# Kernel optimization log

Hardware: AMD Instinct MI355X
Metric: run time of the kernel (lower is better)

Reference implementation:

```python
import jax, jax.numpy as jnp
import numpy as np

N_NODES = 100000


def gcn_conv(x, row, col, norm, W, b):
    # PyG GCNConv: linear transform first, then normalized aggregation.
    h = x @ W                                   # [N, D_out]
    msg = h[col] * norm[:, None]                # gather sources, scale  [E', D_out]
    out = jax.ops.segment_sum(msg, row, num_segments=N_NODES)
    return out + b


def _build_norm(edge_index, n):
    # add self-loops
    loops = jnp.arange(n, dtype=edge_index.dtype)
    row = jnp.concatenate([edge_index[0], loops])  # targets
    col = jnp.concatenate([edge_index[1], loops])  # sources
    deg = jax.ops.segment_sum(jnp.ones(row.shape[0], jnp.float32), row, num_segments=n)
    dinv = jnp.where(deg > 0, jax.lax.rsqrt(deg), 0.0)
    norm = dinv[row] * dinv[col]
    return row, col, norm


def setup_inputs() -> dict:
    key = jax.random.key(0)
    k = jax.random.split(key, 5)
    N, E, IN, H, OUT = N_NODES, 1_600_000, 128, 64, 64
    x = jax.random.normal(k[0], (N, IN), jnp.float32)
    edge_index = jax.random.randint(k[1], (2, E), 0, N, dtype=jnp.int32)
    W1 = jax.random.normal(k[2], (IN, H), jnp.float32) / np.sqrt(IN)
    b1 = jnp.zeros((H,), jnp.float32)
    W2 = jax.random.normal(k[3], (H, OUT), jnp.float32) / np.sqrt(H)
    b2 = jnp.zeros((OUT,), jnp.float32)
    return {"x": x, "edge_index": edge_index, "W1": W1, "b1": b1, "W2": W2, "b2": b2}


def reference(x, edge_index, W1, b1, W2, b2):
    row, col, norm = _build_norm(edge_index, N_NODES)
    h = jax.nn.relu(gcn_conv(x, row, col, norm, W1, b1))
    # dropout is identity in eval mode
    out = gcn_conv(h, row, col, norm, W2, b2)
    return out
```

## Files before the change

kernel.cpp:

```cpp
#include <hip/hip_runtime.h>
#include <hip/hip_bf16.h>
#include <stdint.h>


#define BUCKET_CAP 64
#define GATHER_CAP 58
#define NB_SHIFT 8
#define BIN_W (1 << NB_SHIFT)
#define EPB 4096

typedef __bf16 bf16x8 __attribute__((ext_vector_type(8)));
typedef float  f32x4  __attribute__((ext_vector_type(4)));

__device__ __forceinline__ void prep_w_one(const float* __restrict__ W,
                                           __bf16* __restrict__ Wsw, int t) {
    int lane = t & 63;
    int f = t >> 6;
    int kt = f >> 2, nt = f & 3;
    int k0 = kt * 32 + ((lane >> 4) * 8);
    int n  = nt * 16 + (lane & 15);
    __bf16* dst = Wsw + (size_t)t * 8;
#pragma unroll
    for (int j = 0; j < 8; ++j)
        dst[j] = (__bf16)W[(size_t)(k0 + j) * 64 + n];
}

__global__ void k_binA(const int* __restrict__ row, const int* __restrict__ col,
                       int E, int NB, int NBLK,
                       const float* __restrict__ W1, const float* __restrict__ W2,
                       __bf16* __restrict__ W1sw, __bf16* __restrict__ W2sw,
                       int* __restrict__ lofs_g, int* __restrict__ binbuf) {
    __shared__ int hist[512];
    __shared__ int lofs[512];
    __shared__ int cur[512];
    __shared__ int stage[EPB];
    __shared__ int wsum[4];
    int t = threadIdx.x;
    int blk = blockIdx.x;

    if (blk >= NBLK) {
        int b = blk - NBLK;
        if (b < 4)      prep_w_one(W1, W1sw, b * 256 + t);
        else if (b < 6) prep_w_one(W2, W2sw, (b - 4) * 256 + t);
        return;
    }

    int e0 = blk * EPB;
    int nE = E - e0; if (nE > EPB) nE = EPB;

    for (int i = t; i < 512; i += 256) hist[i] = 0;
    __syncthreads();

    int rr[EPB / 256], cc[EPB / 256];
#pragma unroll
    for (int k = 0; k < EPB / 256; ++k) {
        int idx = k * 256 + t;
        if (idx < nE) {
            rr[k] = row[e0 + idx];
            cc[k] = col[e0 + idx];
            atomicAdd(&hist[((unsigned)rr[k]) >> NB_SHIFT], 1);
        } else rr[k] = -1;
    }
    __syncthreads();

    int h0 = hist[2 * t], h1 = hist[2 * t + 1];
    int s = h0 + h1;
    int v = s;
#pragma unroll
    for (int off = 1; off < 64; off <<= 1) {
        int u = __shfl_up(v, off);
        if ((t & 63) >= off) v += u;
    }
    if ((t & 63) == 63) wsum[t >> 6] = v;
    __syncthreads();
    int wo = 0;
    for (int w = 0; w < (t >> 6); ++w) wo += wsum[w];
    int base = v + wo - s;
    lofs[2 * t]     = base;
    lofs[2 * t + 1] = base + h0;
    cur[2 * t]      = base;
    cur[2 * t + 1]  = base + h0;
    __syncthreads();

#pragma unroll
    for (int k = 0; k < EPB / 256; ++k) {
        if (rr[k] >= 0) {
            int b = ((unsigned)rr[k]) >> NB_SHIFT;
            int p = atomicAdd(&cur[b], 1);
            stage[p] = (cc[k] << NB_SHIFT) | (rr[k] & (BIN_W - 1));
        }
    }
    __syncthreads();

    for (int i = t; i < nE; i += 256)
        binbuf[(size_t)blk * EPB + i] = stage[i];
    for (int i = t; i <= NB; i += 256)
        lofs_g[(size_t)blk * (NB + 1) + i] = lofs[i];
}

#define BB_THREADS 512
__global__ void k_binB(const int* __restrict__ lofs_g, const int* __restrict__ binbuf,
                       int NBLK, int NB, int* __restrict__ cnt, float* __restrict__ dinv,
                       int* __restrict__ bucket, int N) {
    __shared__ int loc[BIN_W];
    int t = threadIdx.x;
    int k = blockIdx.x;
    int node0 = k << NB_SHIFT;

    for (int i = t; i < BIN_W; i += BB_THREADS) loc[i] = 0;
    __syncthreads();

    if (t < NBLK) {
        int s0 = lofs_g[(size_t)t * (NB + 1) + k];
        int s1 = lofs_g[(size_t)t * (NB + 1) + k + 1];
        const int* __restrict__ seg = binbuf + (size_t)t * EPB;
        int i = s0;
        int nxt = (i < s1) ? seg[i] : 0;
        while (i < s1) {
            int v = nxt;
            ++i;
            if (i < s1) nxt = seg[i];
            int rl = v & (BIN_W - 1);
            int c  = (int)(((unsigned)v) >> NB_SHIFT);
            int p = atomicAdd(&loc[rl], 1);
            if (p < BUCKET_CAP)
                bucket[(size_t)(node0 + rl) * BUCKET_CAP + p] = c;
        }
    }
    __syncthreads();

    int node = node0 + t;
    if (t < BIN_W && node < N) {
        int d = loc[t];
        cnt[node] = d;
        dinv[node] = rsqrtf((float)(d + 1));
    }
}

__global__ void k_gemm1(const float* __restrict__ X, const __bf16* __restrict__ W1sw,
                        __bf16* __restrict__ H1, int n_mtiles) {
    constexpr int KT = 4;
    constexpr int M_ITERS = 2;
    constexpr int KDIM = KT * 32;
    int lane = threadIdx.x & 63;
    int wave = threadIdx.x >> 6;
    int task = blockIdx.x * 4 + wave;
    int mt0 = task * M_ITERS;

    bf16x8 Bf[KT * 4];
    const bf16x8* Wv = (const bf16x8*)W1sw;
#pragma unroll
    for (int f = 0; f < KT * 4; ++f)
        Bf[f] = Wv[(size_t)f * 64 + lane];

    int m_in_tile = lane & 15;
    int k0 = (lane >> 4) * 8;

    for (int it = 0; it < M_ITERS; ++it) {
        int mt = mt0 + it;
        if (mt >= n_mtiles) return;
        int node = mt * 16 + m_in_tile;

        bf16x8 Af[KT];
#pragma unroll
        for (int kt = 0; kt < KT; ++kt) {
            const f32x4* p = (const f32x4*)(X + (size_t)node * KDIM + kt * 32 + k0);
            f32x4 lo = p[0], hi = p[1];
            bf16x8 a;
#pragma unroll
            for (int j = 0; j < 4; ++j) {
                a[j]     = (__bf16)lo[j];
                a[j + 4] = (__bf16)hi[j];
            }
            Af[kt] = a;
        }

#pragma unroll
        for (int nt = 0; nt < 4; ++nt) {
            f32x4 c = {0.f, 0.f, 0.f, 0.f};
#pragma unroll
            for (int kt = 0; kt < KT; ++kt)
                c = __builtin_amdgcn_mfma_f32_16x16x32_bf16(Af[kt], Bf[kt * 4 + nt], c, 0, 0, 0);
            int nd = mt * 16 + (lane >> 4) * 4;
            int ft = nt * 16 + (lane & 15);
#pragma unroll
            for (int r = 0; r < 4; ++r)
                H1[(size_t)(nd + r) * 64 + ft] = (__bf16)c[r];
        }
    }
}

__device__ __forceinline__ float tree_reduce8(const float acc8[8], int lane) {
    bool b2 = (lane & 32) != 0;
    float a4[4];
#pragma unroll
    for (int i = 0; i < 4; ++i) {
        float send = b2 ? acc8[i] : acc8[i + 4];
        float keep = b2 ? acc8[i + 4] : acc8[i];
        a4[i] = keep + __shfl_xor(send, 32);
    }
    bool b1 = (lane & 16) != 0;
    float a2[2];
#pragma unroll
    for (int i = 0; i < 2; ++i) {
        float send = b1 ? a4[i] : a4[i + 2];
        float keep = b1 ? a4[i + 2] : a4[i];
        a2[i] = keep + __shfl_xor(send, 16);
    }
    bool b0 = (lane & 8) != 0;
    float send = b0 ? a2[0] : a2[1];
    float keep = b0 ? a2[1] : a2[0];
    return keep + __shfl_xor(send, 8);
}

__device__ __forceinline__ void gather_pair_wide(const __bf16* __restrict__ H,
                                                 const int* __restrict__ cnt,
                                                 const float* __restrict__ dinv,
                                                 const int* __restrict__ bucket,
                                                 int na, int nb, int lane,
                                                 float& sa, float& sb,
                                                 float& dia, float& dib) {
    int dega = cnt[na], degb = cnt[nb];
    int ma = dega > GATHER_CAP ? GATHER_CAP : dega;
    int mb = degb > GATHER_CAP ? GATHER_CAP : degb;
    int   cja = (lane < ma) ? bucket[(size_t)na * BUCKET_CAP + lane] : na;
    int   cjb = (lane < mb) ? bucket[(size_t)nb * BUCKET_CAP + lane] : nb;
    float dja = (lane <= ma) ? dinv[cja] : 0.f;
    float djb = (lane <= mb) ? dinv[cjb] : 0.f;
    dia = dinv[na];
    dib = dinv[nb];

    int r = lane >> 3, g = lane & 7;
    float aa[8] = {0.f, 0.f, 0.f, 0.f, 0.f, 0.f, 0.f, 0.f};
    float ab[8] = {0.f, 0.f, 0.f, 0.f, 0.f, 0.f, 0.f, 0.f};
    int mpa = ma + 1, mpb = mb + 1;

    if (mpa <= 16 && mpb <= 16) {
#pragma unroll
        for (int j = 0; j < 16; j += 8) {
            int   ca = __shfl(cja, j + r);
            float da = __shfl(dja, j + r);
            int   cb = __shfl(cjb, j + r);
            float db = __shfl(djb, j + r);
            bf16x8 ha = *(const bf16x8*)(H + (size_t)ca * 64 + g * 8);
            bf16x8 hb = *(const bf16x8*)(H + (size_t)cb * 64 + g * 8);
#pragma unroll
            for (int i = 0; i < 8; ++i) {
                aa[i] = fmaf(da, (float)ha[i], aa[i]);
                ab[i] = fmaf(db, (float)hb[i], ab[i]);
            }
        }
    } else {
#pragma unroll
        for (int j = 0; j < 32; j += 8) {
            int   ca = __shfl(cja, j + r);
            float da = __shfl(dja, j + r);
            int   cb = __shfl(cjb, j + r);
            float db = __shfl(djb, j + r);
            bf16x8 ha = *(const bf16x8*)(H + (size_t)ca * 64 + g * 8);
            bf16x8 hb = *(const bf16x8*)(H + (size_t)cb * 64 + g * 8);
#pragma unroll
            for (int i = 0; i < 8; ++i) {
                aa[i] = fmaf(da, (float)ha[i], aa[i]);
                ab[i] = fmaf(db, (float)hb[i], ab[i]);
            }
        }
        if (mpa > 32) {
#pragma unroll 1
            for (int j = 32; j < mpa; j += 8) {
                int   c = __shfl(cja, j + r);
                float d = __shfl(dja, j + r);
                bf16x8 h = *(const bf16x8*)(H + (size_t)c * 64 + g * 8);
#pragma unroll
                for (int i = 0; i < 8; ++i)
                    aa[i] = fmaf(d, (float)h[i], aa[i]);
            }
        }
        if (mpb > 32) {
#pragma unroll 1
            for (int j = 32; j < mpb; j += 8) {
                int   c = __shfl(cjb, j + r);
                float d = __shfl(djb, j + r);
                bf16x8 h = *(const bf16x8*)(H + (size_t)c * 64 + g * 8);
#pragma unroll
                for (int i = 0; i < 8; ++i)
                    ab[i] = fmaf(d, (float)h[i], ab[i]);
            }
        }
    }

    sa = tree_reduce8(aa, lane);
    sb = tree_reduce8(ab, lane);
}

__global__ void k_agg1_gemm2(const __bf16* __restrict__ H1, const int* __restrict__ cnt,
                             const float* __restrict__ dinv,
                             const int* __restrict__ bucket, const float* __restrict__ b1,
                             const __bf16* __restrict__ W2sw,
                             __bf16* __restrict__ H2, int N) {
    __shared__ __bf16 G1s[16][72];
    int lane = threadIdx.x & 63;
    int wave = threadIdx.x >> 6;
    int node0 = blockIdx.x * 16;
    int f = (lane & 7) * 8 + (lane >> 3);
    float bias = b1[f];

#pragma unroll
    for (int i = 0; i < 4; i += 2) {
        int nrow = wave * 4 + i;
        int na = node0 + nrow;
        int nb = na + 1;
        int nac = na < N ? na : 0;
        int nbc = nb < N ? nb : 0;
        float sa, sb, dia, dib;
        gather_pair_wide(H1, cnt, dinv, bucket, nac, nbc, lane, sa, sb, dia, dib);
        float va = fmaxf(fmaf(dia, sa, bias), 0.f);
        float vb = fmaxf(fmaf(dib, sb, bias), 0.f);
        if (na >= N) va = 0.f;
        if (nb >= N) vb = 0.f;
        G1s[nrow][f]     = (__bf16)va;
        G1s[nrow + 1][f] = (__bf16)vb;
    }
    __syncthreads();

    int m = lane & 15;
    int k0 = (lane >> 4) * 8;
    const bf16x8* Wv = (const bf16x8*)W2sw;
    bf16x8 Bf0 = Wv[(size_t)(0 * 4 + wave) * 64 + lane];
    bf16x8 Bf1 = Wv[(size_t)(1 * 4 + wave) * 64 + lane];
    bf16x8 Af0 = *(const bf16x8*)&G1s[m][k0];
    bf16x8 Af1 = *(const bf16x8*)&G1s[m][32 + k0];

    f32x4 c = {0.f, 0.f, 0.f, 0.f};
    c = __builtin_amdgcn_mfma_f32_16x16x32_bf16(Af0, Bf0, c, 0, 0, 0);
    c = __builtin_amdgcn_mfma_f32_16x16x32_bf16(Af1, Bf1, c, 0, 0, 0);

    int nd = node0 + (lane >> 4) * 4;
    int ft = wave * 16 + (lane & 15);
#pragma unroll
    for (int r = 0; r < 4; ++r)
        if (nd + r < N)
            H2[(size_t)(nd + r) * 64 + ft] = (__bf16)c[r];
}

__global__ void k_agg2(const __bf16* __restrict__ H2, const int* __restrict__ cnt,
                       const float* __restrict__ dinv,
                       const int* __restrict__ bucket, const float* __restrict__ b2,
                       float* __restrict__ out, int N) {
    int wave = threadIdx.x >> 6;
    int lane = threadIdx.x & 63;
    int na = blockIdx.x * 8 + wave * 2;
    if (na >= N) return;
    int nb = na + 1;
    int nbc = nb < N ? nb : 0;
    int f = (lane & 7) * 8 + (lane >> 3);
    float sa, sb, dia, dib;
    gather_pair_wide(H2, cnt, dinv, bucket, na, nbc, lane, sa, sb, dia, dib);
    float bias = b2[f];
    out[(size_t)na * 64 + f] = fmaf(dia, sa, bias);
    if (nb < N)
        out[(size_t)nb * 64 + f] = fmaf(dib, sb, bias);
}

extern "C" void kernel_launch(void* const* d_in, const int* in_sizes, int n_in,
                              void* d_out, int out_size, void* d_ws, size_t ws_size,
                              hipStream_t stream) {
    (void)n_in; (void)out_size; (void)ws_size;
    const float* x  = (const float*)d_in[0];
    const int*   ei = (const int*)d_in[1];
    const float* W1 = (const float*)d_in[2];
    const float* b1 = (const float*)d_in[3];
    const float* W2 = (const float*)d_in[4];
    const float* b2 = (const float*)d_in[5];

    const int N = in_sizes[0] / 128;
    const int E = in_sizes[1] / 2;
    const int* row = ei;
    const int* col = ei + E;

    const int NB   = (N + BIN_W - 1) >> NB_SHIFT;
    const int NBLK = (E + EPB - 1) / EPB;

    char* ws = (char*)d_ws;
    size_t off = 0;
    auto take = [&](size_t bytes) -> char* {
        char* p = ws + off;
        off += (bytes + 255) & ~(size_t)255;
        return p;
    };
    int*    cnt    = (int*)   take((size_t)N * 4);
    float*  dinv   = (float*) take((size_t)N * 4);
    int*    lofs_g = (int*)   take((size_t)NBLK * (NB + 1) * 4);
    int*    bucket = (int*)   take((size_t)N * BUCKET_CAP * 4);
    __bf16* W1sw   = (__bf16*)take((size_t)16 * 64 * 8 * 2);
    __bf16* W2sw   = (__bf16*)take((size_t)8  * 64 * 8 * 2);
    __bf16* H1     = (__bf16*)take((size_t)N * 64 * 2);
    size_t h2_bytes  = (size_t)N * 64 * 2;
    size_t bin_bytes = (size_t)NBLK * EPB * 4;
    char*   unionbuf = take(h2_bytes > bin_bytes ? h2_bytes : bin_bytes);
    int*    binbuf = (int*)unionbuf;
    __bf16* H2     = (__bf16*)unionbuf;

    const int n_mtiles = (N + 15) / 16;
    const int GB1 = (n_mtiles / 2 + 1 + 3) / 4;

    k_binA<<<NBLK + 6, 256, 0, stream>>>(row, col, E, NB, NBLK,
                                         W1, W2, W1sw, W2sw, lofs_g, binbuf);
    k_binB<<<NB, BB_THREADS, 0, stream>>>(lofs_g, binbuf, NBLK, NB,
                                          cnt, dinv, bucket, N);
    k_gemm1<<<GB1, 256, 0, stream>>>(x, W1sw, H1, n_mtiles);
    k_agg1_gemm2<<<(N + 15) / 16, 256, 0, stream>>>(H1, cnt, dinv, bucket, b1, W2sw, H2, N);
    k_agg2<<<(N + 7) / 8, 256, 0, stream>>>(H2, cnt, dinv, bucket, b2, (float*)d_out, N);
}
```

Measured before the change: 219.3 us.

## Fuse gemm1 into binning kernel and batch gather loads ahead of FMAs

Moves the first GEMM (X@W1) into extra blocks of the binning kernel, so it runs alongside edge binning and one kernel launch goes away. Those gemm blocks convert W1 to bf16 fragments directly from global memory instead of reading the pre-swizzled copy. The aggregation gather now issues all neighbor row loads before the FMAs to expose more memory-level parallelism, at the cost of extra registers. Launch bounds on the aggregation kernels cap register use to keep occupancy up.

```diff
diff --git a/kernel.cpp b/kernel.cpp
--- a/kernel.cpp
+++ b/kernel.cpp
@@ -25,11 +25,13 @@
         dst[j] = (__bf16)W[(size_t)(k0 + j) * 64 + n];
 }
 
-__global__ void k_binA(const int* __restrict__ row, const int* __restrict__ col,
-                       int E, int NB, int NBLK,
-                       const float* __restrict__ W1, const float* __restrict__ W2,
-                       __bf16* __restrict__ W1sw, __bf16* __restrict__ W2sw,
-                       int* __restrict__ lofs_g, int* __restrict__ binbuf) {
+__global__ void k_binA_gemm1(const int* __restrict__ row, const int* __restrict__ col,
+                             int E, int NB, int NBLK,
+                             const float* __restrict__ W1, const float* __restrict__ W2,
+                             __bf16* __restrict__ W1sw, __bf16* __restrict__ W2sw,
+                             int* __restrict__ lofs_g, int* __restrict__ binbuf,
+                             const float* __restrict__ X, __bf16* __restrict__ H1,
+                             int n_mtiles) {
     __shared__ int hist[512];
     __shared__ int lofs[512];
     __shared__ int cur[512];
@@ -37,6 +39,68 @@
     __shared__ int wsum[4];
     int t = threadIdx.x;
     int blk = blockIdx.x;
+
+    if (blk >= NBLK + 6) {
+        constexpr int KT = 4;
+        constexpr int M_ITERS = 2;
+        constexpr int KDIM = KT * 32;
+        int lane = t & 63;
+        int wave = t >> 6;
+        int task = (blk - NBLK - 6) * 4 + wave;
+        int mt0 = task * M_ITERS;
+
+        bf16x8 Bf[KT * 4];
+#pragma unroll
+        for (int kt = 0; kt < KT; ++kt) {
+#pragma unroll
+            for (int nt = 0; nt < 4; ++nt) {
+                int k0 = kt * 32 + ((lane >> 4) * 8);
+                int n  = nt * 16 + (lane & 15);
+                bf16x8 b;
+#pragma unroll
+                for (int j = 0; j < 8; ++j)
+                    b[j] = (__bf16)W1[(size_t)(k0 + j) * 64 + n];
+                Bf[kt * 4 + nt] = b;
+            }
+        }
+
+        int m_in_tile = lane & 15;
+        int k0 = (lane >> 4) * 8;
+
+        for (int it = 0; it < M_ITERS; ++it) {
+            int mt = mt0 + it;
+            if (mt >= n_mtiles) return;
+            int node = mt * 16 + m_in_tile;
+
+            bf16x8 Af[KT];
+#pragma unroll
+            for (int kt = 0; kt < KT; ++kt) {
+                const f32x4* p = (const f32x4*)(X + (size_t)node * KDIM + kt * 32 + k0);
+                f32x4 lo = p[0], hi = p[1];
+                bf16x8 a;
+#pragma unroll
+                for (int j = 0; j < 4; ++j) {
+                    a[j]     = (__bf16)lo[j];
+                    a[j + 4] = (__bf16)hi[j];
+                }
+                Af[kt] = a;
+            }
+
+#pragma unroll
+            for (int nt = 0; nt < 4; ++nt) {
+                f32x4 c = {0.f, 0.f, 0.f, 0.f};
+#pragma unroll
+                for (int kt = 0; kt < KT; ++kt)
+                    c = __builtin_amdgcn_mfma_f32_16x16x32_bf16(Af[kt], Bf[kt * 4 + nt], c, 0, 0, 0);
+                int nd = mt * 16 + (lane >> 4) * 4;
+                int ft = nt * 16 + (lane & 15);
+#pragma unroll
+                for (int r = 0; r < 4; ++r)
+                    H1[(size_t)(nd + r) * 64 + ft] = (__bf16)c[r];
+            }
+        }
+        return;
+    }
 
     if (blk >= NBLK) {
         int b = blk - NBLK;
@@ -134,59 +198,6 @@
         int d = loc[t];
         cnt[node] = d;
         dinv[node] = rsqrtf((float)(d + 1));
-    }
-}
-
-__global__ void k_gemm1(const float* __restrict__ X, const __bf16* __restrict__ W1sw,
-                        __bf16* __restrict__ H1, int n_mtiles) {
-    constexpr int KT = 4;
-    constexpr int M_ITERS = 2;
-    constexpr int KDIM = KT * 32;
-    int lane = threadIdx.x & 63;
-    int wave = threadIdx.x >> 6;
-    int task = blockIdx.x * 4 + wave;
-    int mt0 = task * M_ITERS;
-
-    bf16x8 Bf[KT * 4];
-    const bf16x8* Wv = (const bf16x8*)W1sw;
-#pragma unroll
-    for (int f = 0; f < KT * 4; ++f)
-        Bf[f] = Wv[(size_t)f * 64 + lane];
-
-    int m_in_tile = lane & 15;
-    int k0 = (lane >> 4) * 8;
-
-    for (int it = 0; it < M_ITERS; ++it) {
-        int mt = mt0 + it;
-        if (mt >= n_mtiles) return;
-        int node = mt * 16 + m_in_tile;
-
-        bf16x8 Af[KT];
-#pragma unroll
-        for (int kt = 0; kt < KT; ++kt) {
-            const f32x4* p = (const f32x4*)(X + (size_t)node * KDIM + kt * 32 + k0);
-            f32x4 lo = p[0], hi = p[1];
-            bf16x8 a;
-#pragma unroll
-            for (int j = 0; j < 4; ++j) {
-                a[j]     = (__bf16)lo[j];
-                a[j + 4] = (__bf16)hi[j];
-            }
-            Af[kt] = a;
-        }
-
-#pragma unroll
-        for (int nt = 0; nt < 4; ++nt) {
-            f32x4 c = {0.f, 0.f, 0.f, 0.f};
-#pragma unroll
-            for (int kt = 0; kt < KT; ++kt)
-                c = __builtin_amdgcn_mfma_f32_16x16x32_bf16(Af[kt], Bf[kt * 4 + nt], c, 0, 0, 0);
-            int nd = mt * 16 + (lane >> 4) * 4;
-            int ft = nt * 16 + (lane & 15);
-#pragma unroll
-            for (int r = 0; r < 4; ++r)
-                H1[(size_t)(nd + r) * 64 + ft] = (__bf16)c[r];
-        }
     }
 }
 
@@ -231,38 +242,47 @@
     dib = dinv[nb];
 
     int r = lane >> 3, g = lane & 7;
+    const __bf16* __restrict__ Hg = H + g * 8;
     float aa[8] = {0.f, 0.f, 0.f, 0.f, 0.f, 0.f, 0.f, 0.f};
     float ab[8] = {0.f, 0.f, 0.f, 0.f, 0.f, 0.f, 0.f, 0.f};
     int mpa = ma + 1, mpb = mb + 1;
 
     if (mpa <= 16 && mpb <= 16) {
-#pragma unroll
-        for (int j = 0; j < 16; j += 8) {
-            int   ca = __shfl(cja, j + r);
-            float da = __shfl(dja, j + r);
-            int   cb = __shfl(cjb, j + r);
-            float db = __shfl(djb, j + r);
-            bf16x8 ha = *(const bf16x8*)(H + (size_t)ca * 64 + g * 8);
-            bf16x8 hb = *(const bf16x8*)(H + (size_t)cb * 64 + g * 8);
+        bf16x8 La[2], Lb[2];
+#pragma unroll
+        for (int u = 0; u < 2; ++u) {
+            int ca = __shfl(cja, u * 8 + r);
+            int cb = __shfl(cjb, u * 8 + r);
+            La[u] = *(const bf16x8*)(Hg + (size_t)ca * 64);
+            Lb[u] = *(const bf16x8*)(Hg + (size_t)cb * 64);
+        }
+#pragma unroll
+        for (int u = 0; u < 2; ++u) {
+            float da = __shfl(dja, u * 8 + r);
+            float db = __shfl(djb, u * 8 + r);
 #pragma unroll
             for (int i = 0; i < 8; ++i) {
-                aa[i] = fmaf(da, (float)ha[i], aa[i]);
-                ab[i] = fmaf(db, (float)hb[i], ab[i]);
+                aa[i] = fmaf(da, (float)La[u][i], aa[i]);
+                ab[i] = fmaf(db, (float)Lb[u][i], ab[i]);
             }
         }
     } else {
-#pragma unroll
-        for (int j = 0; j < 32; j += 8) {
-            int   ca = __shfl(cja, j + r);
-            float da = __shfl(dja, j + r);
-            int   cb = __shfl(cjb, j + r);
-            float db = __shfl(djb, j + r);
-            bf16x8 ha = *(const bf16x8*)(H + (size_t)ca * 64 + g * 8);
-            bf16x8 hb = *(const bf16x8*)(H + (size_t)cb * 64 + g * 8);
+        bf16x8 La[4], Lb[4];
+#pragma unroll
+        for (int u = 0; u < 4; ++u) {
+            int ca = __shfl(cja, u * 8 + r);
+            int cb = __shfl(cjb, u * 8 + r);
+            La[u] = *(const bf16x8*)(Hg + (size_t)ca * 64);
+            Lb[u] = *(const bf16x8*)(Hg + (size_t)cb * 64);
+        }
+#pragma unroll
+        for (int u = 0; u < 4; ++u) {
+            float da = __shfl(dja, u * 8 + r);
+            float db = __shfl(djb, u * 8 + r);
 #pragma unroll
             for (int i = 0; i < 8; ++i) {
-                aa[i] = fmaf(da, (float)ha[i], aa[i]);
-                ab[i] = fmaf(db, (float)hb[i], ab[i]);
+                aa[i] = fmaf(da, (float)La[u][i], aa[i]);
+                ab[i] = fmaf(db, (float)Lb[u][i], ab[i]);
             }
         }
         if (mpa > 32) {
@@ -270,7 +290,7 @@
             for (int j = 32; j < mpa; j += 8) {
                 int   c = __shfl(cja, j + r);
                 float d = __shfl(dja, j + r);
-                bf16x8 h = *(const bf16x8*)(H + (size_t)c * 64 + g * 8);
+                bf16x8 h = *(const bf16x8*)(Hg + (size_t)c * 64);
 #pragma unroll
                 for (int i = 0; i < 8; ++i)
                     aa[i] = fmaf(d, (float)h[i], aa[i]);
@@ -281,7 +301,7 @@
             for (int j = 32; j < mpb; j += 8) {
                 int   c = __shfl(cjb, j + r);
                 float d = __shfl(djb, j + r);
-                bf16x8 h = *(const bf16x8*)(H + (size_t)c * 64 + g * 8);
+                bf16x8 h = *(const bf16x8*)(Hg + (size_t)c * 64);
 #pragma unroll
                 for (int i = 0; i < 8; ++i)
                     ab[i] = fmaf(d, (float)h[i], ab[i]);
@@ -293,11 +313,12 @@
     sb = tree_reduce8(ab, lane);
 }
 
-__global__ void k_agg1_gemm2(const __bf16* __restrict__ H1, const int* __restrict__ cnt,
-                             const float* __restrict__ dinv,
-                             const int* __restrict__ bucket, const float* __restrict__ b1,
-                             const __bf16* __restrict__ W2sw,
-                             __bf16* __restrict__ H2, int N) {
+__global__ __launch_bounds__(256, 4)
+void k_agg1_gemm2(const __bf16* __restrict__ H1, const int* __restrict__ cnt,
+                  const float* __restrict__ dinv,
+                  const int* __restrict__ bucket, const float* __restrict__ b1,
+                  const __bf16* __restrict__ W2sw,
+                  __bf16* __restrict__ H2, int N) {
     __shared__ __bf16 G1s[16][72];
     int lane = threadIdx.x & 63;
     int wave = threadIdx.x >> 6;
@@ -343,10 +364,11 @@
             H2[(size_t)(nd + r) * 64 + ft] = (__bf16)c[r];
 }
 
-__global__ void k_agg2(const __bf16* __restrict__ H2, const int* __restrict__ cnt,
-                       const float* __restrict__ dinv,
-                       const int* __restrict__ bucket, const float* __restrict__ b2,
-                       float* __restrict__ out, int N) {
+__global__ __launch_bounds__(256, 4)
+void k_agg2(const __bf16* __restrict__ H2, const int* __restrict__ cnt,
+            const float* __restrict__ dinv,
+            const int* __restrict__ bucket, const float* __restrict__ b2,
+            float* __restrict__ out, int N) {
     int wave = threadIdx.x >> 6;
     int lane = threadIdx.x & 63;
     int na = blockIdx.x * 8 + wave * 2;
@@ -404,11 +426,11 @@
     const int n_mtiles = (N + 15) / 16;
     const int GB1 = (n_mtiles / 2 + 1 + 3) / 4;
 
-    k_binA<<<NBLK + 6, 256, 0, stream>>>(row, col, E, NB, NBLK,
-                                         W1, W2, W1sw, W2sw, lofs_g, binbuf);
+    k_binA_gemm1<<<NBLK + 6 + GB1, 256, 0, stream>>>(row, col, E, NB, NBLK,
+                                                     W1, W2, W1sw, W2sw,
+                                                     lofs_g, binbuf, x, H1, n_mtiles);
     k_binB<<<NB, BB_THREADS, 0, stream>>>(lofs_g, binbuf, NBLK, NB,
                                           cnt, dinv, bucket, N);
-    k_gemm1<<<GB1, 256, 0, stream>>>(x, W1sw, H1, n_mtiles);
     k_agg1_gemm2<<<(N + 15) / 16, 256, 0, stream>>>(H1, cnt, dinv, bucket, b1, W2sw, H2, N);
     k_agg2<<<(N + 7) / 8, 256, 0, stream>>>(H2, cnt, dinv, bucket, b2, (float*)d_out, N);
 }
```

Result: faster. 214.6 us (-2.1%).
